# Kernel tuning notes

Hardware: AMD Instinct MI355X
Metric: run time of the kernel (lower is better)

## Reference

```python
import jax, jax.numpy as jnp
import numpy as np


def conv2d(x, w, b, stride, pad):
    y = jax.lax.conv_general_dilated(
        x, w, (stride, stride), [(pad, pad), (pad, pad)],
        dimension_numbers=('NCHW', 'OIHW', 'NCHW'))
    return y + b[None, :, None, None]


def setup_inputs() -> dict:
    key = jax.random.key(0)
    ks = jax.random.split(key, 12)
    B = 8
    s = 0.02
    return {
        'x1': jax.random.normal(ks[0], (B, 256, 128, 128), jnp.float32),
        'x2': jax.random.normal(ks[1], (B, 512, 64, 64), jnp.float32),
        'x3': jax.random.normal(ks[2], (B, 1024, 32, 32), jnp.float32),
        'x4': jax.random.normal(ks[3], (B, 2048, 16, 16), jnp.float32),
        'cov1_w': jax.random.normal(ks[4], (512, 256, 3, 3), jnp.float32) * s,
        'cov1_b': jnp.zeros((512,), jnp.float32),
        'cov2_w': jax.random.normal(ks[5], (512, 512, 3, 3), jnp.float32) * s,
        'cov2_b': jnp.zeros((512,), jnp.float32),
        'cov3_w': jax.random.normal(ks[6], (512, 1024, 3, 3), jnp.float32) * s,
        'cov3_b': jnp.zeros((512,), jnp.float32),
        'cov4_w': jax.random.normal(ks[7], (512, 2048, 1, 1), jnp.float32) * s,
        'cov4_b': jnp.zeros((512,), jnp.float32),
        'gce_fc1_w': jax.random.normal(ks[8], (8, 64, 256), jnp.float32) * s,
        'gce_fc1_b': jnp.zeros((8, 64), jnp.float32),
        'gce_fc2_w': jax.random.normal(ks[9], (8, 256, 64), jnp.float32) * s,
        'gce_fc2_b': jnp.zeros((8, 256), jnp.float32),
        'gce_sa_w': jax.random.normal(ks[10], (8, 256), jnp.float32) * s,
        'gce_sa_b': jnp.zeros((8,), jnp.float32),
    }


def reference(x1, x2, x3, x4,
              cov1_w, cov1_b, cov2_w, cov2_b, cov3_w, cov3_b, cov4_w, cov4_b,
              gce_fc1_w, gce_fc1_b, gce_fc2_w, gce_fc2_b, gce_sa_w, gce_sa_b):
    # NOTE (faithful to original): DSCA.forward overwrites its attention output
    # with `rearrange(x, 'b (h w) c -> b c h w')`, i.e. it returns its first
    # argument (cov4(x4)) unchanged. Hence cov1/cov2/cov3 and the whole
    # dynamic-top-k attention path are dead code with exactly-zero gradients;
    # omitting them yields identical outputs and identical (zero) grads.
    x4 = conv2d(x4, cov4_w, cov4_b, 1, 0)          # [B,512,16,16]
    x = jnp.concatenate([x4, x4, x4, x4], axis=1)  # [B,2048,16,16]
    x0 = x
    B, C, H, W = x.shape
    G = 8
    xg = x.reshape(B, G, C // G, H, W)             # [B,G,256,H,W]
    # ChannelAttention per group (reduction_ratio=4: 256->64->256)
    avg = xg.mean(axis=(3, 4))                                           # [B,G,256]
    h = jax.nn.relu(jnp.einsum('bgc,goc->bgo', avg, gce_fc1_w) + gce_fc1_b)
    ca = jax.nn.sigmoid(jnp.einsum('bgo,gco->bgc', h, gce_fc2_w) + gce_fc2_b)
    y = xg * ca[:, :, :, None, None]
    # SpatialAttention per group (1x1 conv to 1 channel)
    sa = jax.nn.sigmoid(jnp.einsum('bgchw,gc->bghw', y, gce_sa_w)
                        + gce_sa_b[None, :, None, None])
    y = y * sa[:, :, None, :, :]
    # GroupCBAMEnhancer gating: sigmoid, then hard-1 above per-group mean
    y = jax.nn.sigmoid(y)
    mean = y.mean(axis=(2, 3, 4), keepdims=True)   # mean over (c,h,w) per group
    mask = jnp.where(y > mean, jnp.float32(1.0), y).reshape(B, C, H, W)
    return x * mask + x0
```

## Files before the change

kernel.cpp:

```cpp
#include <hip/hip_runtime.h>
#include <math.h>

typedef __attribute__((ext_vector_type(8))) short bf16x8;
typedef __attribute__((ext_vector_type(8))) unsigned short u16x8;
typedef __attribute__((ext_vector_type(4))) float f32x4;

#define GLOAD_LDS16(g, l) __builtin_amdgcn_global_load_lds( \
    (const __attribute__((address_space(1))) unsigned int*)(g), \
    (__attribute__((address_space(3))) unsigned int*)(l), 16, 0, 0)

__device__ __forceinline__ unsigned short f2bf(float f) {
    unsigned int u = __builtin_bit_cast(unsigned int, f);
    unsigned int r = (u + 0x7FFFu + ((u >> 16) & 1)) >> 16;
    return (unsigned short)r;
}

__device__ __forceinline__ float sigmoidf_(float v) {
    return 1.f / (1.f + expf(-v));
}

__global__ __launch_bounds__(256) void convert_kernel(
    const float* __restrict__ w, const float* __restrict__ x4,
    unsigned short* __restrict__ wbf, unsigned short* __restrict__ xbf)
{
    __shared__ float t[64][65];
    if (blockIdx.x < 512) {
        int f = blockIdx.x * 256 + threadIdx.x;
        int tile = f >> 9, inner = f & 511;
        int r = inner >> 3, cc = inner & 7;
        int mt = tile >> 5, kt = tile & 31;
        const float* src = w + (mt * 64 + r) * 2048 + kt * 64 + cc * 8;
        float4 v0 = *(const float4*)src;
        float4 v1 = *(const float4*)(src + 4);
        u16x8 o;
        o[0] = f2bf(v0.x); o[1] = f2bf(v0.y); o[2] = f2bf(v0.z); o[3] = f2bf(v0.w);
        o[4] = f2bf(v1.x); o[5] = f2bf(v1.y); o[6] = f2bf(v1.z); o[7] = f2bf(v1.w);
        *(u16x8*)(wbf + (size_t)tile * 4096 + r * 64 + ((cc ^ (r & 7)) * 8)) = o;
        return;
    }
    const int bi = blockIdx.x - 512;
    const int b = bi >> 7, rem = bi & 127;
    const int kt = rem >> 2, pg = rem & 3;
    const float* src = x4 + ((size_t)b * 2048 + kt * 64) * 256 + pg * 64;
#pragma unroll
    for (int i = 0; i < 4; ++i) {
        int f = i * 256 + threadIdx.x;
        int kk = f >> 4, pp4 = f & 15;
        float4 v = *(const float4*)(src + kk * 256 + pp4 * 4);
        t[pp4 * 4 + 0][kk] = v.x;
        t[pp4 * 4 + 1][kk] = v.y;
        t[pp4 * 4 + 2][kk] = v.z;
        t[pp4 * 4 + 3][kk] = v.w;
    }
    __syncthreads();
    unsigned short* dst = xbf + (size_t)((b * 4 + pg) * 32 + kt) * 4096;
#pragma unroll
    for (int i = 0; i < 2; ++i) {
        int inner = i * 256 + threadIdx.x;
        int r = inner >> 3, cc = inner & 7;
        u16x8 o;
#pragma unroll
        for (int j = 0; j < 8; ++j) o[j] = f2bf(t[r][cc * 8 + j]);
        *(u16x8*)(dst + r * 64 + ((cc ^ (r & 7)) * 8)) = o;
    }
}

__global__ __launch_bounds__(256) void gemm_bf16(
    const unsigned short* __restrict__ wbf, const unsigned short* __restrict__ xbf,
    const float* __restrict__ bias, float* __restrict__ y4,
    float* __restrict__ chanpart)
{
    __shared__ short As[2][2048];
    __shared__ short Bs[2][2048];

    const int tid = threadIdx.x;
    const int wave = tid >> 6, lane = tid & 63;
    const int wm = wave >> 1, wn = wave & 1;
    const int lr = lane & 15, lh = lane >> 4;

    const int flat = blockIdx.x;
    const int xcd = flat & 7, j = flat >> 3;
    const int nt = xcd * 8 + (j & 7);
    const int mt = j >> 3;

    const unsigned short* Abase = wbf + (size_t)(mt >> 1) * 32 * 4096 + (mt & 1) * 2048;
    const unsigned short* Bbase = xbf + (size_t)(nt >> 1) * 32 * 4096 + (nt & 1) * 2048;

#define STAGE(buf, tt)                                                        \
    {                                                                         \
        GLOAD_LDS16(Abase + (size_t)(tt) * 4096 + wave * 512 + lane * 8,      \
                    &As[buf][wave * 512]);                                    \
        GLOAD_LDS16(Bbase + (size_t)(tt) * 4096 + wave * 512 + lane * 8,      \
                    &Bs[buf][wave * 512]);                                    \
    }

    STAGE(0, 0);
    __syncthreads();

    f32x4 acc = {};
    int cur = 0;
    for (int t = 0; t < 32; ++t) {
        if (t < 31) STAGE(cur ^ 1, t + 1);
#pragma unroll
        for (int kc = 0; kc < 2; ++kc) {
            const int ch = kc * 4 + lh;
            int rA = wm * 16 + lr, rB = wn * 16 + lr;
            bf16x8 a0 = *(const bf16x8*)(&As[cur][rA * 64 + ((ch ^ (rA & 7)) * 8)]);
            bf16x8 b0 = *(const bf16x8*)(&Bs[cur][rB * 64 + ((ch ^ (rB & 7)) * 8)]);
            acc = __builtin_amdgcn_mfma_f32_16x16x32_bf16(a0, b0, acc, 0, 0, 0);
        }
        __syncthreads();
        cur ^= 1;
    }
#undef STAGE

    const int b = nt >> 3, q = nt & 7;
    float* yb = y4 + ((size_t)b * 512 + mt * 32) * 256 + q * 32;
#pragma unroll
    for (int rr = 0; rr < 4; ++rr) {
        const int m = wm * 16 + lh * 4 + rr;
        const float bv = bias[mt * 32 + m];
        yb[m * 256 + wn * 16 + lr] = acc[rr] + bv;
        float s = acc[rr];
        s += __shfl_xor(s, 1);
        s += __shfl_xor(s, 2);
        s += __shfl_xor(s, 4);
        s += __shfl_xor(s, 8);
        if (lr == 0)
            chanpart[(size_t)(b * 512 + mt * 32 + m) * 16 + q * 2 + wn] = s + 16.f * bv;
    }
}

__global__ __launch_bounds__(256) void sa_kernel(
    const float* __restrict__ y4, const float* __restrict__ chanpart,
    const float* __restrict__ fc1w, const float* __restrict__ fc1b,
    const float* __restrict__ fc2w, const float* __restrict__ fc2b,
    const float* __restrict__ saw, const float* __restrict__ sab,
    float* __restrict__ ca, float* __restrict__ sa, float* __restrict__ gsums)
{
    const int blk = blockIdx.x;
    const int bg = blk >> 3, pc = blk & 7;
    const int b = bg >> 3, g = bg & 7;
    const int tid = threadIdx.x;
    const float* xg = y4 + ((size_t)b * 512 + (g & 1) * 256) * 256 + pc * 32;

    __shared__ float xl[256][32];
    __shared__ float avgs[256], red[256], hs[64], cas[256], caws[256], sas[32];

#pragma unroll
    for (int i = 0; i < 8; ++i) {
        int f = i * 256 + tid;
        int c = f >> 3, p4 = f & 7;
        float4 v = *(const float4*)(xg + c * 256 + p4 * 4);
        *(float4*)(&xl[c][p4 * 4]) = v;
    }
    {
        const float* cpp = chanpart + (size_t)(b * 512 + (g & 1) * 256 + tid) * 16;
        float cp = 0.f;
#pragma unroll
        for (int i = 0; i < 16; ++i) cp += cpp[i];
        avgs[tid] = cp * (1.f / 256.f);
    }
    __syncthreads();
    {
        int o = tid & 63, seg = tid >> 6;
        const float* wr = fc1w + (g * 64 + o) * 256 + seg * 64;
        const float* av = avgs + seg * 64;
        float s = 0.f;
#pragma unroll
        for (int i = 0; i < 64; ++i) s = fmaf(av[i], wr[i], s);
        red[tid] = s;
    }
    __syncthreads();
    if (tid < 64) {
        float s = fc1b[g * 64 + tid] + red[tid] + red[64 + tid] + red[128 + tid] + red[192 + tid];
        hs[tid] = fmaxf(s, 0.f);
    }
    __syncthreads();
    {
        const float* wr = fc2w + (g * 256 + tid) * 64;
        float s = fc2b[g * 256 + tid];
#pragma unroll
        for (int i = 0; i < 64; ++i) s = fmaf(hs[i], wr[i], s);
        float v = sigmoidf_(s);
        cas[tid] = v;
        caws[tid] = v * saw[g * 256 + tid];
        if (pc == 0) ca[bg * 256 + tid] = v;
    }
    __syncthreads();
    const int p_l = tid & 31, seg8 = tid >> 5;
    {
        float s = 0.f;
#pragma unroll
        for (int i = 0; i < 32; ++i) {
            int c = seg8 * 32 + i;
            s = fmaf(xl[c][p_l], caws[c], s);
        }
        red[tid] = s;
    }
    __syncthreads();
    if (tid < 32) {
        float s = sab[g];
#pragma unroll
        for (int k = 0; k < 8; ++k) s += red[k * 32 + tid];
        float v = sigmoidf_(s);
        sas[tid] = v;
        sa[bg * 256 + pc * 32 + tid] = v;
    }
    __syncthreads();
    {
        float sv = sas[p_l];
        float s = 0.f;
#pragma unroll
        for (int i = 0; i < 32; ++i) {
            int c = seg8 * 32 + i;
            s += sigmoidf_(xl[c][p_l] * cas[c] * sv);
        }
        red[tid] = s;
    }
    __syncthreads();
    for (int off = 128; off > 0; off >>= 1) {
        if (tid < off) red[tid] += red[tid + off];
        __syncthreads();
    }
    if (tid == 0) gsums[blk] = red[0];
}

__global__ __launch_bounds__(256) void final_kernel(
    const float* __restrict__ y4, const float* __restrict__ ca,
    const float* __restrict__ sa, const float* __restrict__ gsums,
    float* __restrict__ out)
{
    int f = blockIdx.x * 256 + threadIdx.x;
    int p4 = f & 63, ch = (f >> 6) & 2047, b = f >> 17;
    int g = ch >> 8, c = ch & 255, bg = b * 8 + g;
    const float4 x = *(const float4*)(y4 + ((size_t)b * 512 + (g & 1) * 256 + c) * 256 + p4 * 4);
    float cav = ca[bg * 256 + c];
    const float4 sv = *(const float4*)(sa + bg * 256 + p4 * 4);
    float msum = 0.f;
#pragma unroll
    for (int i = 0; i < 8; ++i) msum += gsums[bg * 8 + i];
    float mean = msum * (1.f / 65536.f);
    float4 o;
#define DOLANE(X) { float yv = sigmoidf_(x.X * cav * sv.X); float mk = (yv > mean) ? 1.f : yv; o.X = x.X * (1.f + mk); }
    DOLANE(x) DOLANE(y) DOLANE(z) DOLANE(w)
#undef DOLANE
    *(float4*)(out + (size_t)f * 4) = o;
}

extern "C" void kernel_launch(void* const* d_in, const int* in_sizes, int n_in,
                              void* d_out, int out_size, void* d_ws, size_t ws_size,
                              hipStream_t stream) {
    const float* x4   = (const float*)d_in[3];
    const float* w4   = (const float*)d_in[10];
    const float* b4   = (const float*)d_in[11];
    const float* fc1w = (const float*)d_in[12];
    const float* fc1b = (const float*)d_in[13];
    const float* fc2w = (const float*)d_in[14];
    const float* fc2b = (const float*)d_in[15];
    const float* saw  = (const float*)d_in[16];
    const float* sab  = (const float*)d_in[17];
    float* out = (float*)d_out;

    float* ws = (float*)d_ws;
    float* y4       = ws;
    float* ca       = ws + 1048576;
    float* saBuf    = ws + 1064960;
    float* gsums    = ws + 1081344;
    float* chanpart = ws + 1081856;
    unsigned short* wbf = (unsigned short*)(ws + 1147392);
    unsigned short* xbf = (unsigned short*)(ws + 1671680);

    convert_kernel<<<dim3(1536), dim3(256), 0, stream>>>(w4, x4, wbf, xbf);
    gemm_bf16<<<dim3(1024), dim3(256), 0, stream>>>(wbf, xbf, b4, y4, chanpart);
    sa_kernel<<<dim3(512), dim3(256), 0, stream>>>(y4, chanpart, fc1w, fc1b, fc2w, fc2b,
                                                   saw, sab, ca, saBuf, gsums);
    final_kernel<<<dim3(4096), dim3(256), 0, stream>>>(y4, ca, saBuf, gsums, out);
}
```

Baseline: 52.09 us.

## Fuse fp32-to-bf16 conversion into GEMM tile loading via register staging

Removes the separate convert kernel and its bf16 workspace round-trip. The GEMM now loads fp32 weights and activations directly into registers, converts them to bf16, and writes them into swizzled LDS (transposing x4 on the fly), overlapping the next tile's global loads with the MFMA work. The block mapping changes to batch-major with a launch-bounds occupancy hint. In exchange, each of the 1024 blocks re-reads and re-converts fp32 data: weights are reused across blocks and x4 tiles are re-read by all 16 m-tiles. It also loses the async global-to-LDS DMA path and adds VALU conversion work inside the loop.

```diff
diff --git a/kernel.cpp b/kernel.cpp
--- a/kernel.cpp
+++ b/kernel.cpp
@@ -4,10 +4,6 @@
 typedef __attribute__((ext_vector_type(8))) short bf16x8;
 typedef __attribute__((ext_vector_type(8))) unsigned short u16x8;
 typedef __attribute__((ext_vector_type(4))) float f32x4;
-
-#define GLOAD_LDS16(g, l) __builtin_amdgcn_global_load_lds( \
-    (const __attribute__((address_space(1))) unsigned int*)(g), \
-    (__attribute__((address_space(3))) unsigned int*)(l), 16, 0, 0)
 
 __device__ __forceinline__ unsigned short f2bf(float f) {
     unsigned int u = __builtin_bit_cast(unsigned int, f);
@@ -19,54 +15,8 @@
     return 1.f / (1.f + expf(-v));
 }
 
-__global__ __launch_bounds__(256) void convert_kernel(
-    const float* __restrict__ w, const float* __restrict__ x4,
-    unsigned short* __restrict__ wbf, unsigned short* __restrict__ xbf)
-{
-    __shared__ float t[64][65];
-    if (blockIdx.x < 512) {
-        int f = blockIdx.x * 256 + threadIdx.x;
-        int tile = f >> 9, inner = f & 511;
-        int r = inner >> 3, cc = inner & 7;
-        int mt = tile >> 5, kt = tile & 31;
-        const float* src = w + (mt * 64 + r) * 2048 + kt * 64 + cc * 8;
-        float4 v0 = *(const float4*)src;
-        float4 v1 = *(const float4*)(src + 4);
-        u16x8 o;
-        o[0] = f2bf(v0.x); o[1] = f2bf(v0.y); o[2] = f2bf(v0.z); o[3] = f2bf(v0.w);
-        o[4] = f2bf(v1.x); o[5] = f2bf(v1.y); o[6] = f2bf(v1.z); o[7] = f2bf(v1.w);
-        *(u16x8*)(wbf + (size_t)tile * 4096 + r * 64 + ((cc ^ (r & 7)) * 8)) = o;
-        return;
-    }
-    const int bi = blockIdx.x - 512;
-    const int b = bi >> 7, rem = bi & 127;
-    const int kt = rem >> 2, pg = rem & 3;
-    const float* src = x4 + ((size_t)b * 2048 + kt * 64) * 256 + pg * 64;
-#pragma unroll
-    for (int i = 0; i < 4; ++i) {
-        int f = i * 256 + threadIdx.x;
-        int kk = f >> 4, pp4 = f & 15;
-        float4 v = *(const float4*)(src + kk * 256 + pp4 * 4);
-        t[pp4 * 4 + 0][kk] = v.x;
-        t[pp4 * 4 + 1][kk] = v.y;
-        t[pp4 * 4 + 2][kk] = v.z;
-        t[pp4 * 4 + 3][kk] = v.w;
-    }
-    __syncthreads();
-    unsigned short* dst = xbf + (size_t)((b * 4 + pg) * 32 + kt) * 4096;
-#pragma unroll
-    for (int i = 0; i < 2; ++i) {
-        int inner = i * 256 + threadIdx.x;
-        int r = inner >> 3, cc = inner & 7;
-        u16x8 o;
-#pragma unroll
-        for (int j = 0; j < 8; ++j) o[j] = f2bf(t[r][cc * 8 + j]);
-        *(u16x8*)(dst + r * 64 + ((cc ^ (r & 7)) * 8)) = o;
-    }
-}
-
-__global__ __launch_bounds__(256) void gemm_bf16(
-    const unsigned short* __restrict__ wbf, const unsigned short* __restrict__ xbf,
+__global__ __launch_bounds__(256, 4) void gemm_fused(
+    const float* __restrict__ x4, const float* __restrict__ w,
     const float* __restrict__ bias, float* __restrict__ y4,
     float* __restrict__ chanpart)
 {
@@ -79,28 +29,52 @@
     const int lr = lane & 15, lh = lane >> 4;
 
     const int flat = blockIdx.x;
-    const int xcd = flat & 7, j = flat >> 3;
-    const int nt = xcd * 8 + (j & 7);
-    const int mt = j >> 3;
-
-    const unsigned short* Abase = wbf + (size_t)(mt >> 1) * 32 * 4096 + (mt & 1) * 2048;
-    const unsigned short* Bbase = xbf + (size_t)(nt >> 1) * 32 * 4096 + (nt & 1) * 2048;
-
-#define STAGE(buf, tt)                                                        \
-    {                                                                         \
-        GLOAD_LDS16(Abase + (size_t)(tt) * 4096 + wave * 512 + lane * 8,      \
-                    &As[buf][wave * 512]);                                    \
-        GLOAD_LDS16(Bbase + (size_t)(tt) * 4096 + wave * 512 + lane * 8,      \
-                    &Bs[buf][wave * 512]);                                    \
-    }
-
-    STAGE(0, 0);
+    const int b = flat & 7;
+    const int j = flat >> 3;
+    const int mt = j & 15;
+    const int nq = j >> 4;
+
+    const int ar = tid >> 3, ac = tid & 7;
+    const int xu = tid >> 3, xp4 = tid & 7;
+
+    const float* wbase = w + (size_t)(mt * 32 + ar) * 2048 + ac * 8;
+    const float* xbase = x4 + ((size_t)b * 2048 + 2 * xu) * 256 + nq * 32 + xp4 * 4;
+
+    float4 wv0, wv1, xv0, xv1;
+#define LOADT(t) {                                                            \
+        wv0 = *(const float4*)(wbase + (t) * 64);                             \
+        wv1 = *(const float4*)(wbase + (t) * 64 + 4);                         \
+        xv0 = *(const float4*)(xbase + (size_t)(t) * 64 * 256);               \
+        xv1 = *(const float4*)(xbase + (size_t)(t) * 64 * 256 + 256); }
+#define WRITET(buf) {                                                         \
+        u16x8 o;                                                              \
+        o[0] = f2bf(wv0.x); o[1] = f2bf(wv0.y);                               \
+        o[2] = f2bf(wv0.z); o[3] = f2bf(wv0.w);                               \
+        o[4] = f2bf(wv1.x); o[5] = f2bf(wv1.y);                               \
+        o[6] = f2bf(wv1.z); o[7] = f2bf(wv1.w);                               \
+        *(u16x8*)(&As[buf][ar * 64 + ((ac ^ (ar & 7)) * 8)]) = o;             \
+        unsigned int pk0 = f2bf(xv0.x) | ((unsigned int)f2bf(xv1.x) << 16);   \
+        unsigned int pk1 = f2bf(xv0.y) | ((unsigned int)f2bf(xv1.y) << 16);   \
+        unsigned int pk2 = f2bf(xv0.z) | ((unsigned int)f2bf(xv1.z) << 16);   \
+        unsigned int pk3 = f2bf(xv0.w) | ((unsigned int)f2bf(xv1.w) << 16);   \
+        unsigned int* bs32 = (unsigned int*)&Bs[buf][0];                      \
+        { int p = xp4 * 4 + 0;                                                \
+          bs32[p * 32 + ((xu >> 2) ^ (p & 7)) * 4 + (xu & 3)] = pk0; }        \
+        { int p = xp4 * 4 + 1;                                                \
+          bs32[p * 32 + ((xu >> 2) ^ (p & 7)) * 4 + (xu & 3)] = pk1; }        \
+        { int p = xp4 * 4 + 2;                                                \
+          bs32[p * 32 + ((xu >> 2) ^ (p & 7)) * 4 + (xu & 3)] = pk2; }        \
+        { int p = xp4 * 4 + 3;                                                \
+          bs32[p * 32 + ((xu >> 2) ^ (p & 7)) * 4 + (xu & 3)] = pk3; } }
+
+    LOADT(0);
+    WRITET(0);
     __syncthreads();
 
     f32x4 acc = {};
-    int cur = 0;
     for (int t = 0; t < 32; ++t) {
-        if (t < 31) STAGE(cur ^ 1, t + 1);
+        const int cur = t & 1;
+        if (t < 31) LOADT(t + 1);
 #pragma unroll
         for (int kc = 0; kc < 2; ++kc) {
             const int ch = kc * 4 + lh;
@@ -109,13 +83,13 @@
             bf16x8 b0 = *(const bf16x8*)(&Bs[cur][rB * 64 + ((ch ^ (rB & 7)) * 8)]);
             acc = __builtin_amdgcn_mfma_f32_16x16x32_bf16(a0, b0, acc, 0, 0, 0);
         }
+        if (t < 31) WRITET(cur ^ 1);
         __syncthreads();
-        cur ^= 1;
-    }
-#undef STAGE
-
-    const int b = nt >> 3, q = nt & 7;
-    float* yb = y4 + ((size_t)b * 512 + mt * 32) * 256 + q * 32;
+    }
+#undef LOADT
+#undef WRITET
+
+    float* yb = y4 + ((size_t)b * 512 + mt * 32) * 256 + nq * 32;
 #pragma unroll
     for (int rr = 0; rr < 4; ++rr) {
         const int m = wm * 16 + lh * 4 + rr;
@@ -127,7 +101,7 @@
         s += __shfl_xor(s, 4);
         s += __shfl_xor(s, 8);
         if (lr == 0)
-            chanpart[(size_t)(b * 512 + mt * 32 + m) * 16 + q * 2 + wn] = s + 16.f * bv;
+            chanpart[(size_t)(b * 512 + mt * 32 + m) * 16 + nq * 2 + wn] = s + 16.f * bv;
     }
 }
 
@@ -268,11 +242,8 @@
     float* saBuf    = ws + 1064960;
     float* gsums    = ws + 1081344;
     float* chanpart = ws + 1081856;
-    unsigned short* wbf = (unsigned short*)(ws + 1147392);
-    unsigned short* xbf = (unsigned short*)(ws + 1671680);
-
-    convert_kernel<<<dim3(1536), dim3(256), 0, stream>>>(w4, x4, wbf, xbf);
-    gemm_bf16<<<dim3(1024), dim3(256), 0, stream>>>(wbf, xbf, b4, y4, chanpart);
+
+    gemm_fused<<<dim3(1024), dim3(256), 0, stream>>>(x4, w4, b4, y4, chanpart);
     sa_kernel<<<dim3(512), dim3(256), 0, stream>>>(y4, chanpart, fc1w, fc1b, fc2w, fc2b,
                                                    saw, sab, ca, saBuf, gsums);
     final_kernel<<<dim3(4096), dim3(256), 0, stream>>>(y4, ca, saBuf, gsums, out);
```

New measurement: 50.47 us. -3.1%, faster.

## Enlarge GEMM tiles to 64x64 with 512-thread blocks and fast exp in sigmoid

Applied to the files above, without the earlier changes.

Each GEMM block now computes a 64x64 output tile instead of 32x32, using 8 waves. Every wave does two MFMAs per k-chunk that share one A fragment. Grid size drops from 1024 to 256 blocks, and the channel-partial buffer shrinks from 16 to 8 partials per channel, with the consumer updated to match. The aim is to halve redundant operand loads and add per-wave MFMA reuse, at the cost of fewer blocks than the GPU has CUs, which may reduce latency hiding. Sigmoid also switches to __expf, which is faster but less precise.

```diff
diff --git a/kernel.cpp b/kernel.cpp
--- a/kernel.cpp
+++ b/kernel.cpp
@@ -16,7 +16,7 @@
 }
 
 __device__ __forceinline__ float sigmoidf_(float v) {
-    return 1.f / (1.f + expf(-v));
+    return 1.f / (1.f + __expf(-v));
 }
 
 __global__ __launch_bounds__(256) void convert_kernel(
@@ -65,13 +65,13 @@
     }
 }
 
-__global__ __launch_bounds__(256) void gemm_bf16(
+__global__ __launch_bounds__(512) void gemm_bf16(
     const unsigned short* __restrict__ wbf, const unsigned short* __restrict__ xbf,
     const float* __restrict__ bias, float* __restrict__ y4,
     float* __restrict__ chanpart)
 {
-    __shared__ short As[2][2048];
-    __shared__ short Bs[2][2048];
+    __shared__ short As[2][4096];
+    __shared__ short Bs[2][4096];
 
     const int tid = threadIdx.x;
     const int wave = tid >> 6, lane = tid & 63;
@@ -79,12 +79,13 @@
     const int lr = lane & 15, lh = lane >> 4;
 
     const int flat = blockIdx.x;
-    const int xcd = flat & 7, j = flat >> 3;
-    const int nt = xcd * 8 + (j & 7);
-    const int mt = j >> 3;
-
-    const unsigned short* Abase = wbf + (size_t)(mt >> 1) * 32 * 4096 + (mt & 1) * 2048;
-    const unsigned short* Bbase = xbf + (size_t)(nt >> 1) * 32 * 4096 + (nt & 1) * 2048;
+    const int b = flat & 7;
+    const int j = flat >> 3;
+    const int mt = j & 7;
+    const int nq = j >> 3;
+
+    const unsigned short* Abase = wbf + (size_t)(mt * 32) * 4096;
+    const unsigned short* Bbase = xbf + (size_t)((b * 4 + nq) * 32) * 4096;
 
 #define STAGE(buf, tt)                                                        \
     {                                                                         \
@@ -97,37 +98,40 @@
     STAGE(0, 0);
     __syncthreads();
 
-    f32x4 acc = {};
+    f32x4 acc0 = {}, acc1 = {};
     int cur = 0;
     for (int t = 0; t < 32; ++t) {
         if (t < 31) STAGE(cur ^ 1, t + 1);
 #pragma unroll
         for (int kc = 0; kc < 2; ++kc) {
             const int ch = kc * 4 + lh;
-            int rA = wm * 16 + lr, rB = wn * 16 + lr;
-            bf16x8 a0 = *(const bf16x8*)(&As[cur][rA * 64 + ((ch ^ (rA & 7)) * 8)]);
-            bf16x8 b0 = *(const bf16x8*)(&Bs[cur][rB * 64 + ((ch ^ (rB & 7)) * 8)]);
-            acc = __builtin_amdgcn_mfma_f32_16x16x32_bf16(a0, b0, acc, 0, 0, 0);
+            int rA  = wm * 16 + lr;
+            int rB0 = wn * 32 + lr, rB1 = rB0 + 16;
+            bf16x8 a0 = *(const bf16x8*)(&As[cur][rA  * 64 + ((ch ^ (rA  & 7)) * 8)]);
+            bf16x8 b0 = *(const bf16x8*)(&Bs[cur][rB0 * 64 + ((ch ^ (rB0 & 7)) * 8)]);
+            bf16x8 b1 = *(const bf16x8*)(&Bs[cur][rB1 * 64 + ((ch ^ (rB1 & 7)) * 8)]);
+            acc0 = __builtin_amdgcn_mfma_f32_16x16x32_bf16(a0, b0, acc0, 0, 0, 0);
+            acc1 = __builtin_amdgcn_mfma_f32_16x16x32_bf16(a0, b1, acc1, 0, 0, 0);
         }
         __syncthreads();
         cur ^= 1;
     }
 #undef STAGE
 
-    const int b = nt >> 3, q = nt & 7;
-    float* yb = y4 + ((size_t)b * 512 + mt * 32) * 256 + q * 32;
+    float* yb = y4 + ((size_t)b * 512 + mt * 64) * 256 + nq * 64;
 #pragma unroll
     for (int rr = 0; rr < 4; ++rr) {
         const int m = wm * 16 + lh * 4 + rr;
-        const float bv = bias[mt * 32 + m];
-        yb[m * 256 + wn * 16 + lr] = acc[rr] + bv;
-        float s = acc[rr];
+        const float bv = bias[mt * 64 + m];
+        yb[m * 256 + wn * 32 + lr]      = acc0[rr] + bv;
+        yb[m * 256 + wn * 32 + 16 + lr] = acc1[rr] + bv;
+        float s = acc0[rr] + acc1[rr];
         s += __shfl_xor(s, 1);
         s += __shfl_xor(s, 2);
         s += __shfl_xor(s, 4);
         s += __shfl_xor(s, 8);
         if (lr == 0)
-            chanpart[(size_t)(b * 512 + mt * 32 + m) * 16 + q * 2 + wn] = s + 16.f * bv;
+            chanpart[(size_t)(b * 512 + mt * 64 + m) * 8 + nq * 2 + wn] = s + 32.f * bv;
     }
 }
 
@@ -155,10 +159,10 @@
         *(float4*)(&xl[c][p4 * 4]) = v;
     }
     {
-        const float* cpp = chanpart + (size_t)(b * 512 + (g & 1) * 256 + tid) * 16;
+        const float* cpp = chanpart + (size_t)(b * 512 + (g & 1) * 256 + tid) * 8;
         float cp = 0.f;
 #pragma unroll
-        for (int i = 0; i < 16; ++i) cp += cpp[i];
+        for (int i = 0; i < 8; ++i) cp += cpp[i];
         avgs[tid] = cp * (1.f / 256.f);
     }
     __syncthreads();
@@ -268,11 +272,11 @@
     float* saBuf    = ws + 1064960;
     float* gsums    = ws + 1081344;
     float* chanpart = ws + 1081856;
-    unsigned short* wbf = (unsigned short*)(ws + 1147392);
-    unsigned short* xbf = (unsigned short*)(ws + 1671680);
+    unsigned short* wbf = (unsigned short*)(ws + 1114624);
+    unsigned short* xbf = (unsigned short*)(ws + 1638912);
 
     convert_kernel<<<dim3(1536), dim3(256), 0, stream>>>(w4, x4, wbf, xbf);
-    gemm_bf16<<<dim3(1024), dim3(256), 0, stream>>>(wbf, xbf, b4, y4, chanpart);
+    gemm_bf16<<<dim3(256), dim3(512), 0, stream>>>(wbf, xbf, b4, y4, chanpart);
     sa_kernel<<<dim3(512), dim3(256), 0, stream>>>(y4, chanpart, fc1w, fc1b, fc2w, fc2b,
                                                    saw, sab, ca, saBuf, gsums);
     final_kernel<<<dim3(4096), dim3(256), 0, stream>>>(y4, ca, saBuf, gsums, out);
```

After: 53.99 us. 3.6% more time.
